# Optimization experiments

Hardware: AMD Instinct MI355X
Metric: run time of the kernel (lower is better)

Reference implementation:

```python
import jax, jax.numpy as jnp
import numpy as np

N = 50000    # nodes
R = 3        # relations
E = 600000   # edges per relation
IN, HID, OUT = 128, 64, 64


def setup_inputs() -> dict:
    key = jax.random.key(0)
    k = jax.random.split(key, 5)
    x = jax.random.normal(k[0], (N, IN), dtype=jnp.float32)
    src = jax.random.randint(k[1], (R, E), 0, N, dtype=jnp.int32)
    dst = jax.random.randint(k[2], (R, E), 0, N, dtype=jnp.int32)
    # glorot-ish init like dgl.nn.GraphConv weight; bias init zeros
    W1 = jax.random.normal(k[3], (R, IN, HID), dtype=jnp.float32) * (IN ** -0.5)
    b1 = jnp.zeros((R, HID), dtype=jnp.float32)
    W2 = jax.random.normal(k[4], (R, HID, OUT), dtype=jnp.float32) * (HID ** -0.5)
    b2 = jnp.zeros((R, OUT), dtype=jnp.float32)
    return {"x": x, "W1": W1, "b1": b1, "W2": W2, "b2": b2, "src": src, "dst": dst}


def _graph_conv(x, src, dst, W, b):
    """dgl.nn.GraphConv with norm='both', single relation.
    x: [N, Fin]; src/dst: [E] int; W: [Fin, Fout]; b: [Fout].
    """
    n = x.shape[0]
    ones = jnp.ones(src.shape[0], dtype=x.dtype)
    out_deg = jax.ops.segment_sum(ones, src, num_segments=n)
    h = x * (jnp.maximum(out_deg, 1.0) ** -0.5)[:, None]   # src-side norm
    if W.shape[0] > W.shape[1]:
        # mult W first, then aggregate (fewer flops per edge)
        h = h @ W
        agg = jax.ops.segment_sum(h[src], dst, num_segments=n)  # [N, Fout]
    else:
        agg = jax.ops.segment_sum(h[src], dst, num_segments=n) @ W
    in_deg = jax.ops.segment_sum(ones, dst, num_segments=n)
    return agg * (jnp.maximum(in_deg, 1.0) ** -0.5)[:, None] + b


def _hetero_conv(x, src, dst, W, b):
    # HeteroGraphConv(aggregate='sum'): run each relation's GraphConv, sum results.
    per_rel = jax.vmap(_graph_conv, in_axes=(None, 0, 0, 0, 0))(x, src, dst, W, b)
    return per_rel.sum(axis=0)  # [N, Fout]


def reference(x, W1, b1, W2, b2, src, dst):
    h = jax.nn.relu(_hetero_conv(x, src, dst, W1, b1))
    return _hetero_conv(h, src, dst, W2, b2)
```

## Files before the change

### kernel.cpp

```cpp
#include <hip/hip_runtime.h>

#define NODES 50000
#define RELS  3
#define NEDGE 600000
#define FIN   128
#define FHID  64
#define FOUT  64
#define SEGS  (RELS * NODES)
#define NBLK  ((SEGS + 255) / 256)

#define HC     96
#define HCHUNK (NEDGE / HC)
#define HBYTES NODES
#define HWORDS (HBYTES / 4)

typedef _Float16 half8 __attribute__((ext_vector_type(8)));
typedef float   floatx4 __attribute__((ext_vector_type(4)));

__global__ __launch_bounds__(1024) void hist_kernel(const int* __restrict__ src,
                                                    const int* __restrict__ dst,
                                                    unsigned int* __restrict__ slab32) {
    __shared__ unsigned int bins[HWORDS];
    int chunk = blockIdx.x, job = blockIdx.y;
    const int* arr = (job < 3 ? src + (size_t)job * NEDGE
                              : dst + (size_t)(job - 3) * NEDGE) + (size_t)chunk * HCHUNK;
    for (int w = threadIdx.x; w < HWORDS; w += 1024) bins[w] = 0u;
    __syncthreads();
    for (int i = threadIdx.x; i < HCHUNK; i += 1024) {
        int v = arr[i];
        atomicAdd(&bins[v >> 2], 1u << ((v & 3) * 8));
    }
    __syncthreads();
    unsigned int* out = slab32 + ((size_t)(job * HC + chunk)) * HWORDS;
    for (int w = threadIdx.x; w < HWORDS; w += 1024) out[w] = bins[w];
}

__global__ __launch_bounds__(256) void degnorm_kernel(unsigned char* __restrict__ slab8,
                                                      int* __restrict__ idI,
                                                      float* __restrict__ outnorm,
                                                      float* __restrict__ innorm,
                                                      const float* __restrict__ W1,
                                                      const float* __restrict__ W2,
                                                      _Float16* __restrict__ W1t,
                                                      _Float16* __restrict__ W2t) {
    int gid = blockIdx.x * 256 + threadIdx.x;
    if (gid < 6 * NODES) {
        int j = gid / NODES, b = gid - j * NODES;
        size_t base = (size_t)j * HC * HBYTES + b;
        if (j < 3) {
            int sum = 0;
#pragma unroll 4
            for (int c = 0; c < HC; ++c) sum += slab8[base + (size_t)c * HBYTES];
            outnorm[j * NODES + b] = rsqrtf(fmaxf((float)sum, 1.0f));
        } else {
            int run = 0;
#pragma unroll 4
            for (int c = 0; c < HC; ++c) {
                size_t idx = base + (size_t)c * HBYTES;
                int v = slab8[idx];
                slab8[idx] = (unsigned char)run;
                run += v;
            }
            idI[(j - 3) * NODES + b] = run;
            innorm[(j - 3) * NODES + b] = rsqrtf(fmaxf((float)run, 1.0f));
        }
        return;
    }
    int g2 = gid - 6 * NODES;
    if (g2 < RELS * FIN * FHID) {
        int r = g2 / (FIN * FHID);
        int rem = g2 - r * FIN * FHID;
        int k = rem / FHID, j = rem - k * FHID;
        W1t[((size_t)r * FHID + j) * FIN + k] = (_Float16)W1[g2];
        return;
    }
    int g3 = g2 - RELS * FIN * FHID;
    if (g3 < RELS * FHID * FOUT) {
        int r = g3 / (FHID * FOUT);
        int rem = g3 - r * FHID * FOUT;
        int k = rem / FOUT, j = rem - k * FOUT;
        W2t[((size_t)r * FOUT + j) * FHID + k] = (_Float16)W2[g3];
    }
}

__global__ __launch_bounds__(256) void scan_sums_kernel(const int* __restrict__ idI,
                                                        int* __restrict__ partials) {
    __shared__ int s[256];
    int i = blockIdx.x * 256 + threadIdx.x;
    s[threadIdx.x] = (i < SEGS) ? idI[i] : 0;
    __syncthreads();
    for (int off = 128; off > 0; off >>= 1) {
        if (threadIdx.x < off) s[threadIdx.x] += s[threadIdx.x + off];
        __syncthreads();
    }
    if (threadIdx.x == 0) partials[blockIdx.x] = s[0];
}

__global__ __launch_bounds__(256) void scan_write_kernel(const int* __restrict__ idI,
                                                         const int* __restrict__ partials,
                                                         int* __restrict__ offs) {
    __shared__ int sp[1024];
    __shared__ int s[256];
    int tid = threadIdx.x;
    for (int i = tid; i < 1024; i += 256) sp[i] = (i < NBLK) ? partials[i] : 0;
    __syncthreads();
    for (int off = 1; off < 1024; off <<= 1) {
        int v[4];
#pragma unroll
        for (int k = 0; k < 4; ++k) { int i = tid + k * 256; v[k] = (i >= off) ? sp[i - off] : 0; }
        __syncthreads();
#pragma unroll
        for (int k = 0; k < 4; ++k) sp[tid + k * 256] += v[k];
        __syncthreads();
    }
    int bpre = (blockIdx.x == 0) ? 0 : sp[blockIdx.x - 1];
    int i = blockIdx.x * 256 + tid;
    int v = (i < SEGS) ? idI[i] : 0;
    s[tid] = v;
    __syncthreads();
    for (int off = 1; off < 256; off <<= 1) {
        int t = s[tid];
        int add = (tid >= off) ? s[tid - off] : 0;
        __syncthreads();
        s[tid] = t + add;
        __syncthreads();
    }
    if (i < SEGS) offs[i] = bpre + (s[tid] - v);
}

__global__ __launch_bounds__(1024) void fill2_kernel(const int* __restrict__ src,
                                                     const int* __restrict__ dst,
                                                     const int* __restrict__ offs,
                                                     const unsigned char* __restrict__ slab8,
                                                     unsigned short* __restrict__ edge_src) {
    __shared__ unsigned int cur[HWORDS];
    int chunk = blockIdx.x, r = blockIdx.y;
    for (int w = threadIdx.x; w < HWORDS; w += 1024) cur[w] = 0u;
    __syncthreads();
    size_t ebase = (size_t)r * NEDGE + (size_t)chunk * HCHUNK;
    const unsigned char* pre = slab8 + ((size_t)((3 + r) * HC + chunk)) * HBYTES;
    for (int i = threadIdx.x; i < HCHUNK; i += 1024) {
        int d = dst[ebase + i];
        unsigned int old = atomicAdd(&cur[d >> 2], 1u << ((d & 3) * 8));
        int local = (int)((old >> ((d & 3) * 8)) & 0xffu);
        int pos = offs[r * NODES + d] + (int)pre[d] + local;
        edge_src[pos] = (unsigned short)src[ebase + i];
    }
}

__global__ __launch_bounds__(256, 4) void gemm1_kernel(const float* __restrict__ x,
                                                       const _Float16* __restrict__ W1t,
                                                       const float* __restrict__ outnorm,
                                                       _Float16* __restrict__ h) {
    int lane = threadIdx.x & 63;
    int wv   = threadIdx.x >> 6;
    int m = lane & 15, quad = lane >> 4;
    int n0 = (blockIdx.x * 4 + wv) * 16;
    if (n0 + 16 > NODES) n0 = NODES - 16;
    const float* xrow = x + (size_t)(n0 + m) * FIN + quad * 8;

    floatx4 acc[12];
#pragma unroll
    for (int t = 0; t < 12; ++t) acc[t] = (floatx4){0.f, 0.f, 0.f, 0.f};

#pragma unroll 1
    for (int ks = 0; ks < 4; ++ks) {
        float4 xa = *(const float4*)(xrow + ks * 32);
        float4 xb = *(const float4*)(xrow + ks * 32 + 4);
        half8 a;
        a[0] = (_Float16)xa.x; a[1] = (_Float16)xa.y;
        a[2] = (_Float16)xa.z; a[3] = (_Float16)xa.w;
        a[4] = (_Float16)xb.x; a[5] = (_Float16)xb.y;
        a[6] = (_Float16)xb.z; a[7] = (_Float16)xb.w;
#pragma unroll
        for (int jt = 0; jt < 12; ++jt) {
            const _Float16* bp = W1t + ((size_t)jt * 16 + m) * FIN + ks * 32 + quad * 8;
            half8 b = *(const half8*)bp;
            acc[jt] = __builtin_amdgcn_mfma_f32_16x16x32_f16(a, b, acc[jt], 0, 0, 0);
        }
    }

#pragma unroll
    for (int jt = 0; jt < 12; ++jt) {
        int r = jt >> 2;
        int j = (jt & 3) * 16 + m;
        _Float16* hb = h + (size_t)r * NODES * FHID;
        const float* on = outnorm + r * NODES;
#pragma unroll
        for (int reg = 0; reg < 4; ++reg) {
            int node = n0 + quad * 4 + reg;
            hb[(size_t)node * FHID + j] = (_Float16)(acc[jt][reg] * on[node]);
        }
    }
}

__device__ __forceinline__ void seg_sum8(const _Float16* __restrict__ hb,
                                         const unsigned short* __restrict__ es,
                                         int o, int c, int q, float* __restrict__ s) {
#pragma unroll
    for (int i = 0; i < 8; ++i) s[i] = 0.f;
    int t = 0;
    for (; t + 4 <= c; t += 4) {
        int i0 = es[o + t], i1 = es[o + t + 1], i2 = es[o + t + 2], i3 = es[o + t + 3];
        half8 v0 = *(const half8*)(hb + (size_t)i0 * FHID + q * 8);
        half8 v1 = *(const half8*)(hb + (size_t)i1 * FHID + q * 8);
        half8 v2 = *(const half8*)(hb + (size_t)i2 * FHID + q * 8);
        half8 v3 = *(const half8*)(hb + (size_t)i3 * FHID + q * 8);
#pragma unroll
        for (int i = 0; i < 8; ++i) {
            s[i] += (float)v0[i];
            s[i] += (float)v1[i];
            s[i] += (float)v2[i];
            s[i] += (float)v3[i];
        }
    }
    if (t + 2 <= c) {
        int i0 = es[o + t], i1 = es[o + t + 1];
        half8 v0 = *(const half8*)(hb + (size_t)i0 * FHID + q * 8);
        half8 v1 = *(const half8*)(hb + (size_t)i1 * FHID + q * 8);
#pragma unroll
        for (int i = 0; i < 8; ++i) {
            s[i] += (float)v0[i];
            s[i] += (float)v1[i];
        }
        t += 2;
    }
    if (t < c) {
        int i0 = es[o + t];
        half8 v0 = *(const half8*)(hb + (size_t)i0 * FHID + q * 8);
#pragma unroll
        for (int i = 0; i < 8; ++i) s[i] += (float)v0[i];
    }
}

__global__ __launch_bounds__(256) void gather1_kernel(const _Float16* __restrict__ h,
                                                      const unsigned short* __restrict__ es,
                                                      const int* __restrict__ offs,
                                                      const int* __restrict__ cnt,
                                                      const float* __restrict__ innorm,
                                                      const float* __restrict__ b1,
                                                      _Float16* __restrict__ B) {
    int lane = threadIdx.x & 63;
    int wv   = threadIdx.x >> 6;
    int w    = blockIdx.x * 4 + wv;
    if (w * 8 >= NODES) return;
    int q    = lane & 7;
    int e8   = lane >> 3;
    int d    = w * 8 + e8;
    int c0 = cnt[d], c1 = cnt[NODES + d], c2 = cnt[2 * NODES + d];
    int o0 = offs[d], o1 = offs[NODES + d], o2 = offs[2 * NODES + d];
    float w0 = innorm[d], w1 = innorm[NODES + d], w2 = innorm[2 * NODES + d];

    float tot[8], s[8];
    seg_sum8(h, es, o0, c0, q, s);
#pragma unroll
    for (int i = 0; i < 8; ++i) tot[i] = w0 * s[i];
    seg_sum8(h + (size_t)NODES * FHID, es, o1, c1, q, s);
#pragma unroll
    for (int i = 0; i < 8; ++i) tot[i] = fmaf(w1, s[i], tot[i]);
    seg_sum8(h + 2 * (size_t)NODES * FHID, es, o2, c2, q, s);
#pragma unroll
    for (int i = 0; i < 8; ++i) tot[i] = fmaf(w2, s[i], tot[i]);

    half8 o8;
#pragma unroll
    for (int i = 0; i < 8; ++i) {
        int j = q * 8 + i;
        float bs = b1[j] + b1[FHID + j] + b1[2 * FHID + j];
        o8[i] = (_Float16)fmaxf(tot[i] + bs, 0.f);
    }
    *(half8*)(B + (size_t)d * FHID + q * 8) = o8;
}

__global__ __launch_bounds__(256) void gather2_kernel(const _Float16* __restrict__ h1,
                                                      const unsigned short* __restrict__ es,
                                                      const int* __restrict__ offs,
                                                      const int* __restrict__ cnt,
                                                      const float* __restrict__ outnorm,
                                                      const float* __restrict__ innorm,
                                                      _Float16* __restrict__ A2) {
    int lane = threadIdx.x & 63;
    int wv   = threadIdx.x >> 6;
    int w    = blockIdx.x * 4 + wv;
    int s0   = w * 8;
    if (s0 >= SEGS) return;
    int q    = lane & 7;
    int e8   = lane >> 3;
    int seg  = s0 + e8;
    int o = offs[seg], c = cnt[seg];
    const float* on = outnorm + (s0 / NODES) * NODES;

    float tot[8];
#pragma unroll
    for (int i = 0; i < 8; ++i) tot[i] = 0.f;
    int t = 0;
    for (; t + 4 <= c; t += 4) {
        int i0 = es[o + t], i1 = es[o + t + 1], i2 = es[o + t + 2], i3 = es[o + t + 3];
        float w0 = on[i0], w1 = on[i1], w2 = on[i2], w3 = on[i3];
        half8 v0 = *(const half8*)(h1 + (size_t)i0 * FHID + q * 8);
        half8 v1 = *(const half8*)(h1 + (size_t)i1 * FHID + q * 8);
        half8 v2 = *(const half8*)(h1 + (size_t)i2 * FHID + q * 8);
        half8 v3 = *(const half8*)(h1 + (size_t)i3 * FHID + q * 8);
#pragma unroll
        for (int i = 0; i < 8; ++i) {
            tot[i] = fmaf(w0, (float)v0[i], tot[i]);
            tot[i] = fmaf(w1, (float)v1[i], tot[i]);
            tot[i] = fmaf(w2, (float)v2[i], tot[i]);
            tot[i] = fmaf(w3, (float)v3[i], tot[i]);
        }
    }
    if (t + 2 <= c) {
        int i0 = es[o + t], i1 = es[o + t + 1];
        float w0 = on[i0], w1 = on[i1];
        half8 v0 = *(const half8*)(h1 + (size_t)i0 * FHID + q * 8);
        half8 v1 = *(const half8*)(h1 + (size_t)i1 * FHID + q * 8);
#pragma unroll
        for (int i = 0; i < 8; ++i) {
            tot[i] = fmaf(w0, (float)v0[i], tot[i]);
            tot[i] = fmaf(w1, (float)v1[i], tot[i]);
        }
        t += 2;
    }
    if (t < c) {
        int i0 = es[o + t];
        float w0 = on[i0];
        half8 v0 = *(const half8*)(h1 + (size_t)i0 * FHID + q * 8);
#pragma unroll
        for (int i = 0; i < 8; ++i) tot[i] = fmaf(w0, (float)v0[i], tot[i]);
    }

    float inr = innorm[seg];
    half8 o8;
#pragma unroll
    for (int i = 0; i < 8; ++i) o8[i] = (_Float16)(inr * tot[i]);
    *(half8*)(A2 + (size_t)seg * FHID + q * 8) = o8;
}

__global__ __launch_bounds__(256, 4) void out_kernel(const _Float16* __restrict__ A2,
                                                     const _Float16* __restrict__ W2t,
                                                     const float* __restrict__ b2,
                                                     float* __restrict__ out) {
    int lane = threadIdx.x & 63;
    int wv   = threadIdx.x >> 6;
    int m = lane & 15, quad = lane >> 4;
    int n0 = (blockIdx.x * 4 + wv) * 16;
    if (n0 + 16 > NODES) n0 = NODES - 16;

    floatx4 acc[4];
#pragma unroll
    for (int t = 0; t < 4; ++t) acc[t] = (floatx4){0.f, 0.f, 0.f, 0.f};

#pragma unroll 1
    for (int kk = 0; kk < 6; ++kk) {
        int r = kk >> 1, kb = (kk & 1) * 32;
        const _Float16* ap = A2 + ((size_t)r * NODES + n0 + m) * FHID + kb + quad * 8;
        half8 a = *(const half8*)ap;
#pragma unroll
        for (int jt = 0; jt < 4; ++jt) {
            const _Float16* bp = W2t + ((size_t)(r * FOUT + jt * 16 + m)) * FHID + kb + quad * 8;
            half8 b = *(const half8*)bp;
            acc[jt] = __builtin_amdgcn_mfma_f32_16x16x32_f16(a, b, acc[jt], 0, 0, 0);
        }
    }

#pragma unroll
    for (int jt = 0; jt < 4; ++jt) {
        int j = jt * 16 + m;
        float bs = b2[j] + b2[FOUT + j] + b2[2 * FOUT + j];
#pragma unroll
        for (int reg = 0; reg < 4; ++reg) {
            int node = n0 + quad * 4 + reg;
            out[(size_t)node * FOUT + j] = acc[jt][reg] + bs;
        }
    }
}

extern "C" void kernel_launch(void* const* d_in, const int* in_sizes, int n_in,
                              void* d_out, int out_size, void* d_ws, size_t ws_size,
                              hipStream_t stream) {
    const float* x   = (const float*)d_in[0];
    const float* W1  = (const float*)d_in[1];
    const float* b1  = (const float*)d_in[2];
    const float* W2  = (const float*)d_in[3];
    const float* b2  = (const float*)d_in[4];
    const int*   src = (const int*)d_in[5];
    const int*   dst = (const int*)d_in[6];
    float* out = (float*)d_out;

    int*   idI      = (int*)d_ws;
    int*   offs     = idI + SEGS;
    int*   partials = offs + SEGS;
    unsigned short* edge_src = (unsigned short*)(partials + 1024);
    float* outnorm  = (float*)(edge_src + (size_t)RELS * NEDGE);
    float* innorm   = outnorm + SEGS;
    _Float16* W1t   = (_Float16*)(innorm + SEGS);
    _Float16* W2t   = W1t + (size_t)RELS * FHID * FIN;
    _Float16* h     = W2t + (size_t)RELS * FHID * FOUT;
    _Float16* B     = h + (size_t)SEGS * FHID;
    _Float16* A2    = B + (size_t)NODES * FHID;
    unsigned int*  slab32 = (unsigned int*)h;
    unsigned char* slab8  = (unsigned char*)h;

    const int GW = ((NODES / 16) + 4) / 4;

    hist_kernel<<<dim3(HC, 6), 1024, 0, stream>>>(src, dst, slab32);
    degnorm_kernel<<<(6 * NODES + RELS * FIN * FHID + RELS * FHID * FOUT + 255) / 256,
                     256, 0, stream>>>(slab8, idI, outnorm, innorm, W1, W2, W1t, W2t);
    scan_sums_kernel<<<NBLK, 256, 0, stream>>>(idI, partials);
    scan_write_kernel<<<NBLK, 256, 0, stream>>>(idI, partials, offs);
    fill2_kernel<<<dim3(HC, RELS), 1024, 0, stream>>>(src, dst, offs, slab8, edge_src);

    gemm1_kernel<<<GW, 256, 0, stream>>>(x, W1t, outnorm, h);
    gather1_kernel<<<(NODES / 8 + 3) / 4, 256, 0, stream>>>(h, edge_src, offs, idI, innorm, b1, B);

    gather2_kernel<<<(SEGS / 8 + 3) / 4, 256, 0, stream>>>(B, edge_src, offs, idI, outnorm, innorm, A2);
    out_kernel<<<GW, 256, 0, stream>>>(A2, W2t, b2, out);
}
```

Baseline: 278.2 us.

## Build CSR via two-pass bucketing by destination range instead of per-chunk prefix fill

```diff
diff --git a/kernel.cpp b/kernel.cpp
--- a/kernel.cpp
+++ b/kernel.cpp
@@ -14,14 +14,24 @@
 #define HBYTES NODES
 #define HWORDS (HBYTES / 4)
 
+#define BS     250
+#define NBUK   200
+#define NBUKT  (RELS * NBUK)
+#define CAPLOG 12
+#define CAP    (1 << CAPLOG)
+#define BCH    192
+#define BCHUNK (NEDGE / BCH)
+
 typedef _Float16 half8 __attribute__((ext_vector_type(8)));
 typedef float   floatx4 __attribute__((ext_vector_type(4)));
 
 __global__ __launch_bounds__(1024) void hist_kernel(const int* __restrict__ src,
                                                     const int* __restrict__ dst,
-                                                    unsigned int* __restrict__ slab32) {
+                                                    unsigned int* __restrict__ slab32,
+                                                    int* __restrict__ bcur) {
     __shared__ unsigned int bins[HWORDS];
     int chunk = blockIdx.x, job = blockIdx.y;
+    if (chunk == 0 && job == 0 && threadIdx.x < NBUKT) bcur[threadIdx.x] = 0;
     const int* arr = (job < 3 ? src + (size_t)job * NEDGE
                               : dst + (size_t)(job - 3) * NEDGE) + (size_t)chunk * HCHUNK;
     for (int w = threadIdx.x; w < HWORDS; w += 1024) bins[w] = 0u;
@@ -35,7 +45,36 @@
     for (int w = threadIdx.x; w < HWORDS; w += 1024) out[w] = bins[w];
 }
 
-__global__ __launch_bounds__(256) void degnorm_kernel(unsigned char* __restrict__ slab8,
+__global__ __launch_bounds__(512) void bucketize_kernel(const int* __restrict__ src,
+                                                        const int* __restrict__ dst,
+                                                        int* __restrict__ bcur,
+                                                        unsigned int* __restrict__ rec) {
+    __shared__ unsigned int stage[BCHUNK];
+    __shared__ int bh[NBUK], bbase[NBUK], blc[NBUK];
+    int chunk = blockIdx.x, r = blockIdx.y;
+    for (int i = threadIdx.x; i < NBUK; i += 512) { bh[i] = 0; blc[i] = 0; }
+    __syncthreads();
+    size_t ebase = (size_t)r * NEDGE + (size_t)chunk * BCHUNK;
+    for (int i = threadIdx.x; i < BCHUNK; i += 512) {
+        int d = dst[ebase + i], s = src[ebase + i];
+        int b = d / BS;
+        int dl = d - b * BS;
+        stage[i] = ((unsigned)s << 16) | ((unsigned)b << 8) | (unsigned)dl;
+        atomicAdd(&bh[b], 1);
+    }
+    __syncthreads();
+    for (int i = threadIdx.x; i < NBUK; i += 512)
+        bbase[i] = atomicAdd(&bcur[r * NBUK + i], bh[i]);
+    __syncthreads();
+    for (int i = threadIdx.x; i < BCHUNK; i += 512) {
+        unsigned u = stage[i];
+        int b = (u >> 8) & 255;
+        int slot = bbase[b] + atomicAdd(&blc[b], 1);
+        rec[(((size_t)r * NBUK + b) << CAPLOG) + slot] = u;
+    }
+}
+
+__global__ __launch_bounds__(256) void degnorm_kernel(const unsigned char* __restrict__ slab8,
                                                       int* __restrict__ idI,
                                                       float* __restrict__ outnorm,
                                                       float* __restrict__ innorm,
@@ -47,22 +86,15 @@
     if (gid < 6 * NODES) {
         int j = gid / NODES, b = gid - j * NODES;
         size_t base = (size_t)j * HC * HBYTES + b;
+        int sum = 0;
+#pragma unroll 4
+        for (int c = 0; c < HC; ++c) sum += slab8[base + (size_t)c * HBYTES];
+        float nrm = rsqrtf(fmaxf((float)sum, 1.0f));
         if (j < 3) {
-            int sum = 0;
-#pragma unroll 4
-            for (int c = 0; c < HC; ++c) sum += slab8[base + (size_t)c * HBYTES];
-            outnorm[j * NODES + b] = rsqrtf(fmaxf((float)sum, 1.0f));
+            outnorm[j * NODES + b] = nrm;
         } else {
-            int run = 0;
-#pragma unroll 4
-            for (int c = 0; c < HC; ++c) {
-                size_t idx = base + (size_t)c * HBYTES;
-                int v = slab8[idx];
-                slab8[idx] = (unsigned char)run;
-                run += v;
-            }
-            idI[(j - 3) * NODES + b] = run;
-            innorm[(j - 3) * NODES + b] = rsqrtf(fmaxf((float)run, 1.0f));
+            idI[(j - 3) * NODES + b] = sum;
+            innorm[(j - 3) * NODES + b] = nrm;
         }
         return;
     }
@@ -128,23 +160,26 @@
     if (i < SEGS) offs[i] = bpre + (s[tid] - v);
 }
 
-__global__ __launch_bounds__(1024) void fill2_kernel(const int* __restrict__ src,
-                                                     const int* __restrict__ dst,
-                                                     const int* __restrict__ offs,
-                                                     const unsigned char* __restrict__ slab8,
-                                                     unsigned short* __restrict__ edge_src) {
-    __shared__ unsigned int cur[HWORDS];
-    int chunk = blockIdx.x, r = blockIdx.y;
-    for (int w = threadIdx.x; w < HWORDS; w += 1024) cur[w] = 0u;
-    __syncthreads();
-    size_t ebase = (size_t)r * NEDGE + (size_t)chunk * HCHUNK;
-    const unsigned char* pre = slab8 + ((size_t)((3 + r) * HC + chunk)) * HBYTES;
-    for (int i = threadIdx.x; i < HCHUNK; i += 1024) {
-        int d = dst[ebase + i];
-        unsigned int old = atomicAdd(&cur[d >> 2], 1u << ((d & 3) * 8));
-        int local = (int)((old >> ((d & 3) * 8)) & 0xffu);
-        int pos = offs[r * NODES + d] + (int)pre[d] + local;
-        edge_src[pos] = (unsigned short)src[ebase + i];
+__global__ __launch_bounds__(512) void fillbkt_kernel(const unsigned int* __restrict__ rec,
+                                                      const int* __restrict__ bcur,
+                                                      const int* __restrict__ offs,
+                                                      unsigned short* __restrict__ edge_src) {
+    __shared__ int obase[BS];
+    __shared__ int lcur[BS];
+    int b = blockIdx.x, r = blockIdx.y;
+    int segbase = r * NODES + b * BS;
+    for (int i = threadIdx.x; i < BS; i += 512) {
+        obase[i] = offs[segbase + i];
+        lcur[i] = 0;
+    }
+    __syncthreads();
+    int n = bcur[r * NBUK + b];
+    const unsigned int* rb = rec + (((size_t)r * NBUK + b) << CAPLOG);
+    for (int i = threadIdx.x; i < n; i += 512) {
+        unsigned u = rb[i];
+        int dl = u & 255;
+        int pos = obase[dl] + atomicAdd(&lcur[dl], 1);
+        edge_src[pos] = (unsigned short)(u >> 16);
     }
 }
 
@@ -390,7 +425,8 @@
     int*   idI      = (int*)d_ws;
     int*   offs     = idI + SEGS;
     int*   partials = offs + SEGS;
-    unsigned short* edge_src = (unsigned short*)(partials + 1024);
+    int*   bcur     = partials + 1024;
+    unsigned short* edge_src = (unsigned short*)(bcur + 1024);
     float* outnorm  = (float*)(edge_src + (size_t)RELS * NEDGE);
     float* innorm   = outnorm + SEGS;
     _Float16* W1t   = (_Float16*)(innorm + SEGS);
@@ -400,15 +436,17 @@
     _Float16* A2    = B + (size_t)NODES * FHID;
     unsigned int*  slab32 = (unsigned int*)h;
     unsigned char* slab8  = (unsigned char*)h;
+    unsigned int*  rec    = (unsigned int*)(slab8 + (size_t)6 * HC * HBYTES);
 
     const int GW = ((NODES / 16) + 4) / 4;
 
-    hist_kernel<<<dim3(HC, 6), 1024, 0, stream>>>(src, dst, slab32);
+    hist_kernel<<<dim3(HC, 6), 1024, 0, stream>>>(src, dst, slab32, bcur);
+    bucketize_kernel<<<dim3(BCH, RELS), 512, 0, stream>>>(src, dst, bcur, rec);
     degnorm_kernel<<<(6 * NODES + RELS * FIN * FHID + RELS * FHID * FOUT + 255) / 256,
                      256, 0, stream>>>(slab8, idI, outnorm, innorm, W1, W2, W1t, W2t);
     scan_sums_kernel<<<NBLK, 256, 0, stream>>>(idI, partials);
     scan_write_kernel<<<NBLK, 256, 0, stream>>>(idI, partials, offs);
-    fill2_kernel<<<dim3(HC, RELS), 1024, 0, stream>>>(src, dst, offs, slab8, edge_src);
+    fillbkt_kernel<<<dim3(NBUK, RELS), 512, 0, stream>>>(rec, bcur, offs, edge_src);
 
     gemm1_kernel<<<GW, 256, 0, stream>>>(x, W1t, outnorm, h);
     gather1_kernel<<<(NODES / 8 + 3) / 4, 256, 0, stream>>>(h, edge_src, offs, idI, innorm, b1, B);
```

New measurement: 250.2 us. -10.1%, faster.
